# Kernel optimization log

Hardware: AMD Instinct MI355X
Metric: run time of the kernel (lower is better)

## Reference

```python
import jax, jax.numpy as jnp
import numpy as np

NEG_SLOPE = 0.2
EPS = 1e-16  # PyG softmax denominator epsilon


def gat_conv(x, src, dst, W, a_src, a_dst, bias, concat):
    """PyG-style GATConv (eval mode, self-loops already included in src/dst)."""
    H, D = a_src.shape
    N = x.shape[0]
    h = (x @ W).reshape(N, H, D)                     # [N,H,D]
    alpha_s = jnp.einsum('nhd,hd->nh', h, a_src)     # [N,H]
    alpha_d = jnp.einsum('nhd,hd->nh', h, a_dst)     # [N,H]
    e = alpha_s[src] + alpha_d[dst]                  # [E,H]
    e = jax.nn.leaky_relu(e, NEG_SLOPE)
    # segment softmax over destination nodes
    m = jax.ops.segment_max(e, dst, num_segments=N)  # [N,H]
    m = jax.lax.stop_gradient(m)
    w = jnp.exp(e - m[dst])                          # [E,H]
    denom = jax.ops.segment_sum(w, dst, num_segments=N)  # [N,H]
    a = w / (denom[dst] + EPS)                       # [E,H]
    msg = h[src] * a[:, :, None]                     # [E,H,D]
    out = jax.ops.segment_sum(msg, dst, num_segments=N)  # [N,H,D]
    out = out.reshape(N, H * D) if concat else out.mean(axis=1)
    return out + bias


def setup_inputs() -> dict:
    key = jax.random.key(0)
    ks = jax.random.split(key, 10)
    N, E = 50000, 800000
    F_IN, H, D, C = 256, 4, 64, 64
    HID = H * D  # 256
    x = jax.random.normal(ks[0], (N, F_IN), dtype=jnp.float32)
    edge_index = jax.random.randint(ks[1], (2, E), 0, N, dtype=jnp.int64)
    g = 1.0 / np.sqrt(F_IN)
    W0 = jax.random.normal(ks[2], (F_IN, HID), dtype=jnp.float32) * g
    att_src0 = jax.random.normal(ks[3], (H, D), dtype=jnp.float32) * 0.1
    att_dst0 = jax.random.normal(ks[4], (H, D), dtype=jnp.float32) * 0.1
    b0 = jnp.zeros((HID,), dtype=jnp.float32)
    g2 = 1.0 / np.sqrt(HID)
    W1 = jax.random.normal(ks[5], (HID, C), dtype=jnp.float32) * g2
    att_src1 = jax.random.normal(ks[6], (1, C), dtype=jnp.float32) * 0.1
    att_dst1 = jax.random.normal(ks[7], (1, C), dtype=jnp.float32) * 0.1
    b1 = jnp.zeros((C,), dtype=jnp.float32)
    return {"x": x, "edge_index": edge_index, "W0": W0, "att_src0": att_src0,
            "att_dst0": att_dst0, "b0": b0, "W1": W1, "att_src1": att_src1,
            "att_dst1": att_dst1, "b1": b1}


def reference(x, edge_index, W0, att_src0, att_dst0, b0, W1, att_src1, att_dst1, b1):
    N = x.shape[0]
    loops = jnp.arange(N, dtype=edge_index.dtype)
    src = jnp.concatenate([edge_index[0], loops])  # add self-loops (PyG default)
    dst = jnp.concatenate([edge_index[1], loops])
    # layer 0: concat heads, then ELU (dropout is identity in eval mode)
    h = gat_conv(x, src, dst, W0, att_src0, att_dst0, b0, concat=True)
    h = jax.nn.elu(h)
    # layer 1: single head, no concat (mean over 1 head)
    out = gat_conv(h, src, dst, W1, att_src1, att_dst1, b1, concat=False)
    return out
```

## Files before the change

### kernel.cpp

```cpp
#include <hip/hip_runtime.h>
#include <hip/hip_bf16.h>
#include <math.h>


#define NEG_SLOPE 0.2f
#define CAP0 128
#define CAP1 128

typedef __attribute__((ext_vector_type(8))) short bf16x8;
typedef __attribute__((ext_vector_type(4))) float f32x4;

static __device__ __forceinline__ unsigned f2bf_rne(float f) {
  unsigned u = __float_as_uint(f);
  return (u + 0x7fffu + ((u >> 16) & 1u)) >> 16;
}
static __device__ __forceinline__ float bf2f(unsigned u16) {
  return __uint_as_float(u16 << 16);
}


__global__ void gat_cvt_bf16(const float* __restrict__ in,
                             ushort* __restrict__ out, int n8) {
  int i = blockIdx.x * blockDim.x + threadIdx.x;
  if (i >= n8) return;
  float4 a = *(const float4*)&in[(size_t)i * 8];
  float4 b = *(const float4*)&in[(size_t)i * 8 + 4];
  uint4 o;
  o.x = f2bf_rne(a.x) | (f2bf_rne(a.y) << 16);
  o.y = f2bf_rne(a.z) | (f2bf_rne(a.w) << 16);
  o.z = f2bf_rne(b.x) | (f2bf_rne(b.y) << 16);
  o.w = f2bf_rne(b.z) | (f2bf_rne(b.w) << 16);
  *(uint4*)&out[(size_t)i * 8] = o;
}

__global__ void gat_cvtT_bf16(const float* __restrict__ W,
                              ushort* __restrict__ Wt, int K, int Nw) {
  int i = blockIdx.x * blockDim.x + threadIdx.x;
  if (i >= K * Nw) return;
  int n = i / K, k = i - n * K;
  Wt[i] = (ushort)f2bf_rne(W[(size_t)k * Nw + n]);
}


__global__ void gat_count_kernel(const int* __restrict__ dst, int E, int N,
                                 int* __restrict__ counts) {
  int i = blockIdx.x * blockDim.x + threadIdx.x;
  int ET = E + N;
  if (i >= ET) return;
  int d = (i < E) ? dst[i] : (i - E);
  atomicAdd(&counts[d], 1);
}

__global__ __launch_bounds__(1024) void gat_scan_kernel(
    const int* __restrict__ counts, int* __restrict__ row_off,
    int* __restrict__ cursor, int n) {
  __shared__ int wsum[16];
  __shared__ int s_carry;
  int tid = threadIdx.x;
  int lane = tid & 63;
  int wid = tid >> 6;
  if (tid == 0) s_carry = 0;
  __syncthreads();
  const int TILE = 4096;
  for (int base = 0; base < n; base += TILE) {
    int idx = base + tid * 4;
    int4 v = {0, 0, 0, 0};
    if (idx + 3 < n) {
      v = *(const int4*)&counts[idx];
    } else {
      if (idx + 0 < n) v.x = counts[idx + 0];
      if (idx + 1 < n) v.y = counts[idx + 1];
      if (idx + 2 < n) v.z = counts[idx + 2];
      if (idx + 3 < n) v.w = counts[idx + 3];
    }
    int t0 = v.x, t1 = t0 + v.y, t2 = t1 + v.z, t3 = t2 + v.w;
    int x = t3;
    #pragma unroll
    for (int off = 1; off < 64; off <<= 1) {
      int y = __shfl_up(x, off, 64);
      if (lane >= off) x += y;
    }
    if (lane == 63) wsum[wid] = x;
    __syncthreads();
    if (tid < 16) {
      int s = wsum[tid];
      #pragma unroll
      for (int off = 1; off < 16; off <<= 1) {
        int y = __shfl_up(s, off, 16);
        if (tid >= off) s += y;
      }
      wsum[tid] = s;
    }
    __syncthreads();
    int carry = s_carry;
    int excl_wave = (wid > 0) ? wsum[wid - 1] : 0;
    int b = carry + excl_wave + (x - t3);
    if (idx + 0 < n) { row_off[idx + 0] = b;      cursor[idx + 0] = b;      }
    if (idx + 1 < n) { row_off[idx + 1] = b + t0; cursor[idx + 1] = b + t0; }
    if (idx + 2 < n) { row_off[idx + 2] = b + t1; cursor[idx + 2] = b + t1; }
    if (idx + 3 < n) { row_off[idx + 3] = b + t2; cursor[idx + 3] = b + t2; }
    __syncthreads();
    if (tid == 1023) s_carry = b + t3;
    __syncthreads();
  }
  if (threadIdx.x == 0) row_off[n] = s_carry;
}

__global__ void gat_fill_kernel(const int* __restrict__ src,
                                const int* __restrict__ dst, int E, int N,
                                int* __restrict__ cursor, int* __restrict__ col) {
  int i = blockIdx.x * blockDim.x + threadIdx.x;
  int ET = E + N;
  if (i >= ET) return;
  int s, d;
  if (i < E) { s = src[i]; d = dst[i]; }
  else       { s = d = i - E; }
  int pos = atomicAdd(&cursor[d], 1);
  col[pos] = s;
}


template <int BN, int WM, int WN, bool WRITE_F32, bool WRITE_BF16>
__global__ __launch_bounds__(256) void gat_gemm_bf16(
    const ushort* __restrict__ A, const ushort* __restrict__ Bt,
    float* __restrict__ C, ushort* __restrict__ Cb, int M, int K, int N) {
  constexpr int BM = 128, BK = 32;
  constexpr int MR = WM / 16, NR = WN / 16;
  constexpr int WCOLS = BN / WN;
  __shared__ __align__(16) ushort Al[BM][40];
  __shared__ __align__(16) ushort Bl[BN][40];
  int tid = threadIdx.x;
  int lane = tid & 63, wid = tid >> 6;
  int wrow = (wid / WCOLS) * WM, wcol = (wid % WCOLS) * WN;
  int brow = blockIdx.x * BM, bcol = blockIdx.y * BN;
  int r0 = tid >> 2, seg = tid & 3;
  int kg = lane >> 4, rl = lane & 15;
  f32x4 acc[MR][NR] = {};
  for (int k0 = 0; k0 < K; k0 += BK) {
    #pragma unroll
    for (int h = 0; h < BM / 64; ++h) {
      int row = r0 + h * 64;
      int ar = brow + row;
      uint4 v = make_uint4(0u, 0u, 0u, 0u);
      if (ar < M) v = *(const uint4*)&A[(size_t)ar * K + k0 + seg * 8];
      *(uint4*)&Al[row][seg * 8] = v;
    }
    #pragma unroll
    for (int h = 0; h < BN / 64; ++h) {
      int row = r0 + h * 64;
      uint4 v = *(const uint4*)&Bt[(size_t)(bcol + row) * K + k0 + seg * 8];
      *(uint4*)&Bl[row][seg * 8] = v;
    }
    __syncthreads();
    bf16x8 af[MR], bfr[NR];
    #pragma unroll
    for (int m = 0; m < MR; ++m)
      af[m] = *(const bf16x8*)&Al[wrow + m * 16 + rl][kg * 8];
    #pragma unroll
    for (int n = 0; n < NR; ++n)
      bfr[n] = *(const bf16x8*)&Bl[wcol + n * 16 + rl][kg * 8];
    #pragma unroll
    for (int m = 0; m < MR; ++m)
      #pragma unroll
      for (int n = 0; n < NR; ++n)
        acc[m][n] = __builtin_amdgcn_mfma_f32_16x16x32_bf16(
            af[m], bfr[n], acc[m][n], 0, 0, 0);
    __syncthreads();
  }
  int orow = kg * 4;
  #pragma unroll
  for (int m = 0; m < MR; ++m) {
    #pragma unroll
    for (int j = 0; j < 4; ++j) {
      int r = brow + wrow + m * 16 + orow + j;
      if (r < M) {
        #pragma unroll
        for (int n = 0; n < NR; ++n) {
          int c = bcol + wcol + n * 16 + rl;
          float v = acc[m][n][j];
          if constexpr (WRITE_F32) C[(size_t)r * N + c] = v;
          if constexpr (WRITE_BF16) Cb[(size_t)r * N + c] = (ushort)f2bf_rne(v);
        }
      }
    }
  }
}


__global__ __launch_bounds__(256) void gat_alpha_b_kernel(
    const ushort* __restrict__ hb, const float* __restrict__ a_src,
    const float* __restrict__ a_dst, float* __restrict__ as_out,
    float* __restrict__ ad_out, int N, int H) {
  int lane = threadIdx.x & 63;
  int wid = threadIdx.x >> 6;
  int g = blockIdx.x * 4 + wid;
  if (g >= N * H) return;
  int hh = g % H;
  float v = bf2f(hb[(size_t)g * 64 + lane]);
  float s = v * a_src[hh * 64 + lane];
  float d = v * a_dst[hh * 64 + lane];
  #pragma unroll
  for (int off = 32; off; off >>= 1) {
    s += __shfl_xor(s, off, 64);
    d += __shfl_xor(d, off, 64);
  }
  if (lane == 0) {
    as_out[g] = s;
    ad_out[g] = d;
  }
}

__global__ __launch_bounds__(256) void gat_alpha_kernel(
    const float* __restrict__ h, const float* __restrict__ a_src,
    const float* __restrict__ a_dst, float* __restrict__ as_out,
    float* __restrict__ ad_out, int N, int H) {
  int lane = threadIdx.x & 63;
  int wid = threadIdx.x >> 6;
  int g = blockIdx.x * 4 + wid;
  if (g >= N * H) return;
  int hh = g % H;
  float v = h[(size_t)g * 64 + lane];
  float s = v * a_src[hh * 64 + lane];
  float d = v * a_dst[hh * 64 + lane];
  #pragma unroll
  for (int off = 32; off; off >>= 1) {
    s += __shfl_xor(s, off, 64);
    d += __shfl_xor(d, off, 64);
  }
  if (lane == 0) {
    as_out[g] = s;
    ad_out[g] = d;
  }
}


__global__ __launch_bounds__(256) void gat_agg0_kernel(
    const unsigned* __restrict__ h0b, const float* __restrict__ as,
    const float* __restrict__ ad, const int* __restrict__ row_off,
    const int* __restrict__ col, const float* __restrict__ bias,
    ushort* __restrict__ x1b, int N) {
  __shared__ int scol[4][CAP0];
  __shared__ float wt[4][CAP0][4];
  int lane = threadIdx.x & 63;
  int wid = threadIdx.x >> 6;
  int n = blockIdx.x * 4 + wid;
  if (n >= N) return;
  int beg = row_off[n];
  int deg = row_off[n + 1] - beg;
  int degc = deg < CAP0 ? deg : CAP0;
  for (int jj = lane; jj < degc; jj += 64) scol[wid][jj] = col[beg + jj];

  int q = lane >> 4, slot = lane & 15;
  float adv = ad[n * 4 + q];

  float m = -INFINITY;
  for (int jj = slot; jj < deg; jj += 16) {
    int s = (jj < CAP0) ? scol[wid][jj] : col[beg + jj];
    float e = as[s * 4 + q] + adv;
    e = (e > 0.f) ? e : NEG_SLOPE * e;
    if (jj < CAP0) wt[wid][jj][q] = e;
    m = fmaxf(m, e);
  }
  #pragma unroll
  for (int off = 8; off; off >>= 1) m = fmaxf(m, __shfl_xor(m, off, 64));

  float dsum = 0.f;
  for (int jj = slot; jj < deg; jj += 16) {
    float e;
    if (jj < CAP0) {
      e = wt[wid][jj][q];
    } else {
      int s = col[beg + jj];
      e = as[s * 4 + q] + adv;
      e = (e > 0.f) ? e : NEG_SLOPE * e;
    }
    float w = __expf(e - m);
    if (jj < CAP0) wt[wid][jj][q] = w;
    dsum += w;
  }
  #pragma unroll
  for (int off = 8; off; off >>= 1) dsum += __shfl_xor(dsum, off, 64);
  float inv = 1.f / (dsum + 1e-16f);

  float4 acc = make_float4(0.f, 0.f, 0.f, 0.f);
  int c2 = lane * 2;
  if (deg <= CAP0) {
    int jj = 0;
    for (; jj + 4 <= deg; jj += 4) {
      int s0 = __builtin_amdgcn_readfirstlane(scol[wid][jj + 0]);
      int s1 = __builtin_amdgcn_readfirstlane(scol[wid][jj + 1]);
      int s2 = __builtin_amdgcn_readfirstlane(scol[wid][jj + 2]);
      int s3 = __builtin_amdgcn_readfirstlane(scol[wid][jj + 3]);
      uint2 v0 = *(const uint2*)(h0b + (size_t)s0 * 128 + c2);
      uint2 v1 = *(const uint2*)(h0b + (size_t)s1 * 128 + c2);
      uint2 v2 = *(const uint2*)(h0b + (size_t)s2 * 128 + c2);
      uint2 v3 = *(const uint2*)(h0b + (size_t)s3 * 128 + c2);
      float w0 = wt[wid][jj + 0][q];
      float w1 = wt[wid][jj + 1][q];
      float w2 = wt[wid][jj + 2][q];
      float w3 = wt[wid][jj + 3][q];
      acc.x = fmaf(w0, __uint_as_float(v0.x << 16), acc.x);
      acc.y = fmaf(w0, __uint_as_float(v0.x & 0xffff0000u), acc.y);
      acc.z = fmaf(w0, __uint_as_float(v0.y << 16), acc.z);
      acc.w = fmaf(w0, __uint_as_float(v0.y & 0xffff0000u), acc.w);
      acc.x = fmaf(w1, __uint_as_float(v1.x << 16), acc.x);
      acc.y = fmaf(w1, __uint_as_float(v1.x & 0xffff0000u), acc.y);
      acc.z = fmaf(w1, __uint_as_float(v1.y << 16), acc.z);
      acc.w = fmaf(w1, __uint_as_float(v1.y & 0xffff0000u), acc.w);
      acc.x = fmaf(w2, __uint_as_float(v2.x << 16), acc.x);
      acc.y = fmaf(w2, __uint_as_float(v2.x & 0xffff0000u), acc.y);
      acc.z = fmaf(w2, __uint_as_float(v2.y << 16), acc.z);
      acc.w = fmaf(w2, __uint_as_float(v2.y & 0xffff0000u), acc.w);
      acc.x = fmaf(w3, __uint_as_float(v3.x << 16), acc.x);
      acc.y = fmaf(w3, __uint_as_float(v3.x & 0xffff0000u), acc.y);
      acc.z = fmaf(w3, __uint_as_float(v3.y << 16), acc.z);
      acc.w = fmaf(w3, __uint_as_float(v3.y & 0xffff0000u), acc.w);
    }
    for (; jj < deg; ++jj) {
      int s = __builtin_amdgcn_readfirstlane(scol[wid][jj]);
      uint2 v = *(const uint2*)(h0b + (size_t)s * 128 + c2);
      float w = wt[wid][jj][q];
      acc.x = fmaf(w, __uint_as_float(v.x << 16), acc.x);
      acc.y = fmaf(w, __uint_as_float(v.x & 0xffff0000u), acc.y);
      acc.z = fmaf(w, __uint_as_float(v.y << 16), acc.z);
      acc.w = fmaf(w, __uint_as_float(v.y & 0xffff0000u), acc.w);
    }
  } else {
    for (int jj = 0; jj < deg; ++jj) {
      int s = (jj < CAP0) ? scol[wid][jj] : col[beg + jj];
      s = __builtin_amdgcn_readfirstlane(s);
      uint2 v = *(const uint2*)(h0b + (size_t)s * 128 + c2);
      float w;
      if (jj < CAP0) {
        w = wt[wid][jj][q];
      } else {
        float e = as[s * 4 + q] + adv;
        e = (e > 0.f) ? e : NEG_SLOPE * e;
        w = __expf(e - m);
      }
      acc.x = fmaf(w, __uint_as_float(v.x << 16), acc.x);
      acc.y = fmaf(w, __uint_as_float(v.x & 0xffff0000u), acc.y);
      acc.z = fmaf(w, __uint_as_float(v.y << 16), acc.z);
      acc.w = fmaf(w, __uint_as_float(v.y & 0xffff0000u), acc.w);
    }
  }

  int c0 = lane * 4;
  float4 bv = *(const float4*)&bias[c0];
  float o0 = acc.x * inv + bv.x;
  float o1 = acc.y * inv + bv.y;
  float o2 = acc.z * inv + bv.z;
  float o3 = acc.w * inv + bv.w;
  o0 = (o0 > 0.f) ? o0 : (__expf(o0) - 1.f);
  o1 = (o1 > 0.f) ? o1 : (__expf(o1) - 1.f);
  o2 = (o2 > 0.f) ? o2 : (__expf(o2) - 1.f);
  o3 = (o3 > 0.f) ? o3 : (__expf(o3) - 1.f);
  uint2 p;
  p.x = f2bf_rne(o0) | (f2bf_rne(o1) << 16);
  p.y = f2bf_rne(o2) | (f2bf_rne(o3) << 16);
  *(uint2*)&x1b[(size_t)n * 256 + c0] = p;
}


__global__ __launch_bounds__(256) void gat_agg1_kernel(
    const float* __restrict__ h1, const float* __restrict__ as,
    const float* __restrict__ ad, const int* __restrict__ row_off,
    const int* __restrict__ col, const float* __restrict__ bias,
    float* __restrict__ out, int N) {
  __shared__ int scol[4][CAP1];
  __shared__ float wt[4][CAP1];
  int lane = threadIdx.x & 63;
  int wid = threadIdx.x >> 6;
  int n = blockIdx.x * 4 + wid;
  if (n >= N) return;
  int beg = row_off[n];
  int deg = row_off[n + 1] - beg;
  int degc = deg < CAP1 ? deg : CAP1;
  for (int jj = lane; jj < degc; jj += 64) scol[wid][jj] = col[beg + jj];
  float adv = ad[n];

  float m = -INFINITY;
  for (int jj = lane; jj < deg; jj += 64) {
    int s = (jj < CAP1) ? scol[wid][jj] : col[beg + jj];
    float e = as[s] + adv;
    e = (e > 0.f) ? e : NEG_SLOPE * e;
    if (jj < CAP1) wt[wid][jj] = e;
    m = fmaxf(m, e);
  }
  #pragma unroll
  for (int off = 32; off; off >>= 1) m = fmaxf(m, __shfl_xor(m, off, 64));

  float dsum = 0.f;
  for (int jj = lane; jj < deg; jj += 64) {
    float e;
    if (jj < CAP1) {
      e = wt[wid][jj];
    } else {
      int s = col[beg + jj];
      e = as[s] + adv;
      e = (e > 0.f) ? e : NEG_SLOPE * e;
    }
    float w = __expf(e - m);
    if (jj < CAP1) wt[wid][jj] = w;
    dsum += w;
  }
  #pragma unroll
  for (int off = 32; off; off >>= 1) dsum += __shfl_xor(dsum, off, 64);
  float inv = 1.f / (dsum + 1e-16f);

  float acc = 0.f;
  if (deg <= CAP1) {
    int jj = 0;
    for (; jj + 4 <= deg; jj += 4) {
      int s0 = __builtin_amdgcn_readfirstlane(scol[wid][jj + 0]);
      int s1 = __builtin_amdgcn_readfirstlane(scol[wid][jj + 1]);
      int s2 = __builtin_amdgcn_readfirstlane(scol[wid][jj + 2]);
      int s3 = __builtin_amdgcn_readfirstlane(scol[wid][jj + 3]);
      float v0 = h1[(size_t)s0 * 64 + lane];
      float v1 = h1[(size_t)s1 * 64 + lane];
      float v2 = h1[(size_t)s2 * 64 + lane];
      float v3 = h1[(size_t)s3 * 64 + lane];
      acc = fmaf(wt[wid][jj + 0], v0, acc);
      acc = fmaf(wt[wid][jj + 1], v1, acc);
      acc = fmaf(wt[wid][jj + 2], v2, acc);
      acc = fmaf(wt[wid][jj + 3], v3, acc);
    }
    for (; jj < deg; ++jj) {
      int s = __builtin_amdgcn_readfirstlane(scol[wid][jj]);
      acc = fmaf(wt[wid][jj], h1[(size_t)s * 64 + lane], acc);
    }
  } else {
    for (int jj = 0; jj < deg; ++jj) {
      int s = (jj < CAP1) ? scol[wid][jj] : col[beg + jj];
      s = __builtin_amdgcn_readfirstlane(s);
      float v = h1[(size_t)s * 64 + lane];
      float w;
      if (jj < CAP1) {
        w = wt[wid][jj];
      } else {
        float e = as[s] + adv;
        e = (e > 0.f) ? e : NEG_SLOPE * e;
        w = __expf(e - m);
      }
      acc = fmaf(w, v, acc);
    }
  }
  out[(size_t)n * 64 + lane] = acc * inv + bias[lane];
}


extern "C" void kernel_launch(void* const* d_in, const int* in_sizes, int n_in,
                              void* d_out, int out_size, void* d_ws, size_t ws_size,
                              hipStream_t stream) {
  const float* x        = (const float*)d_in[0];
  const int*   eidx     = (const int*)d_in[1];
  const float* W0       = (const float*)d_in[2];
  const float* att_src0 = (const float*)d_in[3];
  const float* att_dst0 = (const float*)d_in[4];
  const float* b0       = (const float*)d_in[5];
  const float* W1       = (const float*)d_in[6];
  const float* att_src1 = (const float*)d_in[7];
  const float* att_dst1 = (const float*)d_in[8];
  const float* b1       = (const float*)d_in[9];
  float* out = (float*)d_out;

  const int F_IN = 256, HID = 256, H = 4, C = 64;
  const int N = in_sizes[0] / F_IN;
  const int E = in_sizes[1] / 2;
  const int ET = E + N;

  const int* src = eidx;
  const int* dst = eidx + E;

  char* w = (char*)d_ws;
  auto take = [&](size_t bytes) {
    char* p = w;
    w += (bytes + 255) & ~(size_t)255;
    return p;
  };
  ushort* xb      = (ushort*)take((size_t)N * F_IN * 2);
  ushort* W0t     = (ushort*)take((size_t)F_IN * HID * 2);
  ushort* W1t     = (ushort*)take((size_t)HID * C * 2);
  ushort* h0b     = (ushort*)take((size_t)N * HID * 2);
  ushort* x1b     = (ushort*)take((size_t)N * HID * 2);
  float*  h1      = (float*)take((size_t)N * C * 4);
  float*  as0     = (float*)take((size_t)N * H * 4);
  float*  ad0     = (float*)take((size_t)N * H * 4);
  float*  as1     = (float*)take((size_t)N * 4);
  float*  ad1     = (float*)take((size_t)N * 4);
  int*    row_off = (int*)take((size_t)(N + 1) * 4);
  int*    cursor  = (int*)take((size_t)N * 4);
  int*    counts  = (int*)take((size_t)N * 4);
  int*    col     = (int*)take((size_t)ET * 4);

  {
    int n8 = N * F_IN / 8;
    gat_cvt_bf16<<<(n8 + 255) / 256, 256, 0, stream>>>(x, xb, n8);
    gat_cvtT_bf16<<<(F_IN * HID + 255) / 256, 256, 0, stream>>>(W0, W0t, F_IN, HID);
    gat_cvtT_bf16<<<(HID * C + 255) / 256, 256, 0, stream>>>(W1, W1t, HID, C);
  }

  hipMemsetAsync(counts, 0, (size_t)N * 4, stream);
  {
    int blocks = (ET + 255) / 256;
    gat_count_kernel<<<blocks, 256, 0, stream>>>(dst, E, N, counts);
    gat_scan_kernel<<<1, 1024, 0, stream>>>(counts, row_off, cursor, N);
    gat_fill_kernel<<<blocks, 256, 0, stream>>>(src, dst, E, N, cursor, col);
  }

  {
    dim3 grid((N + 127) / 128, HID / 128);
    gat_gemm_bf16<128, 64, 64, false, true>
        <<<grid, 256, 0, stream>>>(xb, W0t, nullptr, h0b, N, F_IN, HID);
  }
  {
    int blocks = (N * H + 3) / 4;
    gat_alpha_b_kernel<<<blocks, 256, 0, stream>>>(h0b, att_src0, att_dst0,
                                                   as0, ad0, N, H);
  }
  gat_agg0_kernel<<<(N + 3) / 4, 256, 0, stream>>>((const unsigned*)h0b, as0,
                                                   ad0, row_off, col, b0, x1b, N);

  {
    dim3 grid((N + 127) / 128, C / 64);
    gat_gemm_bf16<64, 32, 64, true, false>
        <<<grid, 256, 0, stream>>>(x1b, W1t, h1, nullptr, N, HID, C);
  }
  {
    int blocks = (N * 1 + 3) / 4;
    gat_alpha_kernel<<<blocks, 256, 0, stream>>>(h1, att_src1, att_dst1,
                                                 as1, ad1, N, 1);
  }
  gat_agg1_kernel<<<(N + 3) / 4, 256, 0, stream>>>(h1, as1, ad1, row_off, col,
                                                   b1, out, N);
}
```

Measured before the change: 325.0 us.

## Fuse attention logits into GEMM epilogue, store layer-1 features in bf16, unroll gathers

The attention logit dot products are now computed in the GEMM epilogue from the fp32 accumulators, using shuffle reductions across the 16-lane column groups. This removes both separate alpha kernels and the re-read of h they required. Layer-1 features are stored as bf16 instead of fp32, halving gather traffic in the second aggregation, and both aggregation kernels unroll the neighbour gather by 8 instead of 4 to keep more loads in flight. In exchange, layer-1 features lose precision, and the logits now come from unrounded accumulators, so they differ slightly from before.

```diff
diff --git a/kernel.cpp b/kernel.cpp
--- a/kernel.cpp
+++ b/kernel.cpp
@@ -16,6 +16,12 @@
 }
 static __device__ __forceinline__ float bf2f(unsigned u16) {
   return __uint_as_float(u16 << 16);
+}
+static __device__ __forceinline__ void fma4(float4& acc, float w, uint2 v) {
+  acc.x = fmaf(w, __uint_as_float(v.x << 16), acc.x);
+  acc.y = fmaf(w, __uint_as_float(v.x & 0xffff0000u), acc.y);
+  acc.z = fmaf(w, __uint_as_float(v.y << 16), acc.z);
+  acc.w = fmaf(w, __uint_as_float(v.y & 0xffff0000u), acc.w);
 }
 
 
@@ -120,10 +126,12 @@
 }
 
 
-template <int BN, int WM, int WN, bool WRITE_F32, bool WRITE_BF16>
+template <int BN, int WM, int WN, bool WRITE_F32, bool WRITE_BF16, bool ALPHA>
 __global__ __launch_bounds__(256) void gat_gemm_bf16(
     const ushort* __restrict__ A, const ushort* __restrict__ Bt,
-    float* __restrict__ C, ushort* __restrict__ Cb, int M, int K, int N) {
+    float* __restrict__ C, ushort* __restrict__ Cb, int M, int K, int N,
+    const float* __restrict__ a_src, const float* __restrict__ a_dst,
+    float* __restrict__ as_out, float* __restrict__ ad_out, int H) {
   constexpr int BM = 128, BK = 32;
   constexpr int MR = WM / 16, NR = WN / 16;
   constexpr int WCOLS = BN / WN;
@@ -184,52 +192,37 @@
       }
     }
   }
-}
-
-
-__global__ __launch_bounds__(256) void gat_alpha_b_kernel(
-    const ushort* __restrict__ hb, const float* __restrict__ a_src,
-    const float* __restrict__ a_dst, float* __restrict__ as_out,
-    float* __restrict__ ad_out, int N, int H) {
-  int lane = threadIdx.x & 63;
-  int wid = threadIdx.x >> 6;
-  int g = blockIdx.x * 4 + wid;
-  if (g >= N * H) return;
-  int hh = g % H;
-  float v = bf2f(hb[(size_t)g * 64 + lane]);
-  float s = v * a_src[hh * 64 + lane];
-  float d = v * a_dst[hh * 64 + lane];
-  #pragma unroll
-  for (int off = 32; off; off >>= 1) {
-    s += __shfl_xor(s, off, 64);
-    d += __shfl_xor(d, off, 64);
-  }
-  if (lane == 0) {
-    as_out[g] = s;
-    ad_out[g] = d;
-  }
-}
-
-__global__ __launch_bounds__(256) void gat_alpha_kernel(
-    const float* __restrict__ h, const float* __restrict__ a_src,
-    const float* __restrict__ a_dst, float* __restrict__ as_out,
-    float* __restrict__ ad_out, int N, int H) {
-  int lane = threadIdx.x & 63;
-  int wid = threadIdx.x >> 6;
-  int g = blockIdx.x * 4 + wid;
-  if (g >= N * H) return;
-  int hh = g % H;
-  float v = h[(size_t)g * 64 + lane];
-  float s = v * a_src[hh * 64 + lane];
-  float d = v * a_dst[hh * 64 + lane];
-  #pragma unroll
-  for (int off = 32; off; off >>= 1) {
-    s += __shfl_xor(s, off, 64);
-    d += __shfl_xor(d, off, 64);
-  }
-  if (lane == 0) {
-    as_out[g] = s;
-    ad_out[g] = d;
+  if constexpr (ALPHA) {
+    static_assert(WN == 64, "alpha fusion needs one head per wave");
+    int hh = (bcol + wcol) >> 6;
+    float asv[NR], adv[NR];
+    #pragma unroll
+    for (int n = 0; n < NR; ++n) {
+      asv[n] = a_src[hh * 64 + n * 16 + rl];
+      adv[n] = a_dst[hh * 64 + n * 16 + rl];
+    }
+    #pragma unroll
+    for (int m = 0; m < MR; ++m) {
+      #pragma unroll
+      for (int j = 0; j < 4; ++j) {
+        float ps = 0.f, pd = 0.f;
+        #pragma unroll
+        for (int n = 0; n < NR; ++n) {
+          ps = fmaf(acc[m][n][j], asv[n], ps);
+          pd = fmaf(acc[m][n][j], adv[n], pd);
+        }
+        #pragma unroll
+        for (int off = 1; off < 16; off <<= 1) {
+          ps += __shfl_xor(ps, off, 64);
+          pd += __shfl_xor(pd, off, 64);
+        }
+        int r = brow + wrow + m * 16 + orow + j;
+        if (rl == 0 && r < M) {
+          as_out[(size_t)r * H + hh] = ps;
+          ad_out[(size_t)r * H + hh] = pd;
+        }
+      }
+    }
   }
 }
 
@@ -286,44 +279,38 @@
   int c2 = lane * 2;
   if (deg <= CAP0) {
     int jj = 0;
-    for (; jj + 4 <= deg; jj += 4) {
+    for (; jj + 8 <= deg; jj += 8) {
       int s0 = __builtin_amdgcn_readfirstlane(scol[wid][jj + 0]);
       int s1 = __builtin_amdgcn_readfirstlane(scol[wid][jj + 1]);
       int s2 = __builtin_amdgcn_readfirstlane(scol[wid][jj + 2]);
       int s3 = __builtin_amdgcn_readfirstlane(scol[wid][jj + 3]);
+      int s4 = __builtin_amdgcn_readfirstlane(scol[wid][jj + 4]);
+      int s5 = __builtin_amdgcn_readfirstlane(scol[wid][jj + 5]);
+      int s6 = __builtin_amdgcn_readfirstlane(scol[wid][jj + 6]);
+      int s7 = __builtin_amdgcn_readfirstlane(scol[wid][jj + 7]);
       uint2 v0 = *(const uint2*)(h0b + (size_t)s0 * 128 + c2);
       uint2 v1 = *(const uint2*)(h0b + (size_t)s1 * 128 + c2);
       uint2 v2 = *(const uint2*)(h0b + (size_t)s2 * 128 + c2);
       uint2 v3 = *(const uint2*)(h0b + (size_t)s3 * 128 + c2);
+      uint2 v4 = *(const uint2*)(h0b + (size_t)s4 * 128 + c2);
+      uint2 v5 = *(const uint2*)(h0b + (size_t)s5 * 128 + c2);
+      uint2 v6 = *(const uint2*)(h0b + (size_t)s6 * 128 + c2);
+      uint2 v7 = *(const uint2*)(h0b + (size_t)s7 * 128 + c2);
       float w0 = wt[wid][jj + 0][q];
       float w1 = wt[wid][jj + 1][q];
       float w2 = wt[wid][jj + 2][q];
       float w3 = wt[wid][jj + 3][q];
-      acc.x = fmaf(w0, __uint_as_float(v0.x << 16), acc.x);
-      acc.y = fmaf(w0, __uint_as_float(v0.x & 0xffff0000u), acc.y);
-      acc.z = fmaf(w0, __uint_as_float(v0.y << 16), acc.z);
-      acc.w = fmaf(w0, __uint_as_float(v0.y & 0xffff0000u), acc.w);
-      acc.x = fmaf(w1, __uint_as_float(v1.x << 16), acc.x);
-      acc.y = fmaf(w1, __uint_as_float(v1.x & 0xffff0000u), acc.y);
-      acc.z = fmaf(w1, __uint_as_float(v1.y << 16), acc.z);
-      acc.w = fmaf(w1, __uint_as_float(v1.y & 0xffff0000u), acc.w);
-      acc.x = fmaf(w2, __uint_as_float(v2.x << 16), acc.x);
-      acc.y = fmaf(w2, __uint_as_float(v2.x & 0xffff0000u), acc.y);
-      acc.z = fmaf(w2, __uint_as_float(v2.y << 16), acc.z);
-      acc.w = fmaf(w2, __uint_as_float(v2.y & 0xffff0000u), acc.w);
-      acc.x = fmaf(w3, __uint_as_float(v3.x << 16), acc.x);
-      acc.y = fmaf(w3, __uint_as_float(v3.x & 0xffff0000u), acc.y);
-      acc.z = fmaf(w3, __uint_as_float(v3.y << 16), acc.z);
-      acc.w = fmaf(w3, __uint_as_float(v3.y & 0xffff0000u), acc.w);
+      float w4 = wt[wid][jj + 4][q];
+      float w5 = wt[wid][jj + 5][q];
+      float w6 = wt[wid][jj + 6][q];
+      float w7 = wt[wid][jj + 7][q];
+      fma4(acc, w0, v0); fma4(acc, w1, v1); fma4(acc, w2, v2); fma4(acc, w3, v3);
+      fma4(acc, w4, v4); fma4(acc, w5, v5); fma4(acc, w6, v6); fma4(acc, w7, v7);
     }
     for (; jj < deg; ++jj) {
       int s = __builtin_amdgcn_readfirstlane(scol[wid][jj]);
       uint2 v = *(const uint2*)(h0b + (size_t)s * 128 + c2);
-      float w = wt[wid][jj][q];
-      acc.x = fmaf(w, __uint_as_float(v.x << 16), acc.x);
-      acc.y = fmaf(w, __uint_as_float(v.x & 0xffff0000u), acc.y);
-      acc.z = fmaf(w, __uint_as_float(v.y << 16), acc.z);
-      acc.w = fmaf(w, __uint_as_float(v.y & 0xffff0000u), acc.w);
+      fma4(acc, wt[wid][jj][q], v);
     }
   } else {
     for (int jj = 0; jj < deg; ++jj) {
@@ -338,10 +325,7 @@
         e = (e > 0.f) ? e : NEG_SLOPE * e;
         w = __expf(e - m);
       }
-      acc.x = fmaf(w, __uint_as_float(v.x << 16), acc.x);
-      acc.y = fmaf(w, __uint_as_float(v.x & 0xffff0000u), acc.y);
-      acc.z = fmaf(w, __uint_as_float(v.y << 16), acc.z);
-      acc.w = fmaf(w, __uint_as_float(v.y & 0xffff0000u), acc.w);
+      fma4(acc, w, v);
     }
   }
 
@@ -363,7 +347,7 @@
 
 
 __global__ __launch_bounds__(256) void gat_agg1_kernel(
-    const float* __restrict__ h1, const float* __restrict__ as,
+    const ushort* __restrict__ h1b, const float* __restrict__ as,
     const float* __restrict__ ad, const int* __restrict__ row_off,
     const int* __restrict__ col, const float* __restrict__ bias,
     float* __restrict__ out, int N) {
@@ -411,29 +395,41 @@
   float acc = 0.f;
   if (deg <= CAP1) {
     int jj = 0;
-    for (; jj + 4 <= deg; jj += 4) {
+    for (; jj + 8 <= deg; jj += 8) {
       int s0 = __builtin_amdgcn_readfirstlane(scol[wid][jj + 0]);
       int s1 = __builtin_amdgcn_readfirstlane(scol[wid][jj + 1]);
       int s2 = __builtin_amdgcn_readfirstlane(scol[wid][jj + 2]);
       int s3 = __builtin_amdgcn_readfirstlane(scol[wid][jj + 3]);
-      float v0 = h1[(size_t)s0 * 64 + lane];
-      float v1 = h1[(size_t)s1 * 64 + lane];
-      float v2 = h1[(size_t)s2 * 64 + lane];
-      float v3 = h1[(size_t)s3 * 64 + lane];
+      int s4 = __builtin_amdgcn_readfirstlane(scol[wid][jj + 4]);
+      int s5 = __builtin_amdgcn_readfirstlane(scol[wid][jj + 5]);
+      int s6 = __builtin_amdgcn_readfirstlane(scol[wid][jj + 6]);
+      int s7 = __builtin_amdgcn_readfirstlane(scol[wid][jj + 7]);
+      float v0 = bf2f(h1b[(size_t)s0 * 64 + lane]);
+      float v1 = bf2f(h1b[(size_t)s1 * 64 + lane]);
+      float v2 = bf2f(h1b[(size_t)s2 * 64 + lane]);
+      float v3 = bf2f(h1b[(size_t)s3 * 64 + lane]);
+      float v4 = bf2f(h1b[(size_t)s4 * 64 + lane]);
+      float v5 = bf2f(h1b[(size_t)s5 * 64 + lane]);
+      float v6 = bf2f(h1b[(size_t)s6 * 64 + lane]);
+      float v7 = bf2f(h1b[(size_t)s7 * 64 + lane]);
       acc = fmaf(wt[wid][jj + 0], v0, acc);
       acc = fmaf(wt[wid][jj + 1], v1, acc);
       acc = fmaf(wt[wid][jj + 2], v2, acc);
       acc = fmaf(wt[wid][jj + 3], v3, acc);
+      acc = fmaf(wt[wid][jj + 4], v4, acc);
+      acc = fmaf(wt[wid][jj + 5], v5, acc);
+      acc = fmaf(wt[wid][jj + 6], v6, acc);
+      acc = fmaf(wt[wid][jj + 7], v7, acc);
     }
     for (; jj < deg; ++jj) {
       int s = __builtin_amdgcn_readfirstlane(scol[wid][jj]);
-      acc = fmaf(wt[wid][jj], h1[(size_t)s * 64 + lane], acc);
+      acc = fmaf(wt[wid][jj], bf2f(h1b[(size_t)s * 64 + lane]), acc);
     }
   } else {
     for (int jj = 0; jj < deg; ++jj) {
       int s = (jj < CAP1) ? scol[wid][jj] : col[beg + jj];
       s = __builtin_amdgcn_readfirstlane(s);
-      float v = h1[(size_t)s * 64 + lane];
+      float v = bf2f(h1b[(size_t)s * 64 + lane]);
       float w;
       if (jj < CAP1) {
         w = wt[wid][jj];
@@ -483,7 +479,7 @@
   ushort* W1t     = (ushort*)take((size_t)HID * C * 2);
   ushort* h0b     = (ushort*)take((size_t)N * HID * 2);
   ushort* x1b     = (ushort*)take((size_t)N * HID * 2);
-  float*  h1      = (float*)take((size_t)N * C * 4);
+  ushort* h1b     = (ushort*)take((size_t)N * C * 2);
   float*  as0     = (float*)take((size_t)N * H * 4);
   float*  ad0     = (float*)take((size_t)N * H * 4);
   float*  as1     = (float*)take((size_t)N * 4);
@@ -500,7 +496,7 @@
     gat_cvtT_bf16<<<(HID * C + 255) / 256, 256, 0, stream>>>(W1, W1t, HID, C);
   }
 
-  hipMemsetAsync(counts, 0, (size_t)N * 4, stream);
+  (void)hipMemsetAsync(counts, 0, (size_t)N * 4, stream);
   {
     int blocks = (ET + 255) / 256;
     gat_count_kernel<<<blocks, 256, 0, stream>>>(dst, E, N, counts);
@@ -510,27 +506,19 @@
 
   {
     dim3 grid((N + 127) / 128, HID / 128);
-    gat_gemm_bf16<128, 64, 64, false, true>
-        <<<grid, 256, 0, stream>>>(xb, W0t, nullptr, h0b, N, F_IN, HID);
-  }
-  {
-    int blocks = (N * H + 3) / 4;
-    gat_alpha_b_kernel<<<blocks, 256, 0, stream>>>(h0b, att_src0, att_dst0,
-                                                   as0, ad0, N, H);
+    gat_gemm_bf16<128, 64, 64, false, true, true>
+        <<<grid, 256, 0, stream>>>(xb, W0t, nullptr, h0b, N, F_IN, HID,
+                                   att_src0, att_dst0, as0, ad0, H);
   }
   gat_agg0_kernel<<<(N + 3) / 4, 256, 0, stream>>>((const unsigned*)h0b, as0,
                                                    ad0, row_off, col, b0, x1b, N);
 
   {
     dim3 grid((N + 127) / 128, C / 64);
-    gat_gemm_bf16<64, 32, 64, true, false>
-        <<<grid, 256, 0, stream>>>(x1b, W1t, h1, nullptr, N, HID, C);
-  }
-  {
-    int blocks = (N * 1 + 3) / 4;
-    gat_alpha_kernel<<<blocks, 256, 0, stream>>>(h1, att_src1, att_dst1,
-                                                 as1, ad1, N, 1);
-  }
-  gat_agg1_kernel<<<(N + 3) / 4, 256, 0, stream>>>(h1, as1, ad1, row_off, col,
+    gat_gemm_bf16<64, 32, 64, false, true, true>
+        <<<grid, 256, 0, stream>>>(x1b, W1t, nullptr, h1b, N, HID, C,
+                                   att_src1, att_dst1, as1, ad1, 1);
+  }
+  gat_agg1_kernel<<<(N + 3) / 4, 256, 0, stream>>>(h1b, as1, ad1, row_off, col,
                                                    b1, out, N);
 }
```

Result: faster. 280.7 us (-13.6%).
